# Kernel tuning notes

Hardware: AMD Instinct MI355X
Metric: run time of the kernel (lower is better)

Reference implementation:

```python
import jax, jax.numpy as jnp
import numpy as np

TEMPERATURE = 34.0
PAD = 1  # kernel_size // 2

def setup_inputs() -> dict:
    key = jax.random.key(0)
    ks = jax.random.split(key, 5)
    B, C, H, W = 32, 256, 56, 56
    K, O, I, kh = 4, 256, 256, 3
    hidden = int(C * 0.25) + 1  # 65
    return {
        "x": jax.random.normal(ks[0], (B, C, H, W), jnp.float32),
        "fc1_w": jax.random.normal(ks[1], (hidden, C), jnp.float32) * (2.0 / C) ** 0.5,
        "fc2_w": jax.random.normal(ks[2], (K, hidden), jnp.float32) * (2.0 / hidden) ** 0.5,
        "fc2_b": jnp.zeros((K,), jnp.float32),
        "weight": jax.random.normal(ks[3], (K, O, I, kh, kh), jnp.float32) * (2.0 / (I * kh * kh)) ** 0.5,
        "bias": jnp.zeros((K, O), jnp.float32),
    }

def reference(x, fc1_w, fc2_w, fc2_b, weight, bias):
    # attention2d: global avg pool -> 1x1 conv (fc1) -> relu -> 1x1 conv (fc2) -> softmax(logits/T)
    pooled = x.mean(axis=(2, 3))                      # [B, C]
    h = jax.nn.relu(pooled @ fc1_w.T)                 # [B, hidden]
    logits = h @ fc2_w.T + fc2_b                      # [B, K]
    att = jax.nn.softmax(logits / TEMPERATURE, axis=1)
    # aggregate per-sample conv weights/bias over K kernel banks
    agg_w = jnp.einsum('bk,koihw->boihw', att, weight)  # [B, O, I, kh, kw]
    agg_b = att @ bias                                  # [B, O]
    # per-sample conv (torch emulates via groups=B): vmap over batch
    def conv_one(xi, wi):
        return jax.lax.conv_general_dilated(
            xi[None], wi, window_strides=(1, 1),
            padding=((PAD, PAD), (PAD, PAD)),
            dimension_numbers=('NCHW', 'OIHW', 'NCHW'))[0]
    out = jax.vmap(conv_one)(x, agg_w)                 # [B, O, H, W]
    return out + agg_b[:, :, None, None]
```

## Files before the change

kernel.cpp:

```cpp
#include <hip/hip_runtime.h>


typedef short bf16x8 __attribute__((ext_vector_type(8)));
typedef float f32x16 __attribute__((ext_vector_type(16)));

__device__ __forceinline__ unsigned short f2bf(float f) {
  unsigned int u = __float_as_uint(f);
  return (unsigned short)((u + 0x7FFFu + ((u >> 16) & 1u)) >> 16);
}
__device__ __forceinline__ float bf2f(unsigned short h) {
  return __uint_as_float(((unsigned int)h) << 16);
}

__global__ void xcast_k(const float* __restrict__ x, unsigned short* __restrict__ xb,
                        float* __restrict__ pooled) {
  __shared__ __align__(16) unsigned short tile[64 * 260];
  int b = blockIdx.y;
  int hw0 = blockIdx.x * 64;
  int t = threadIdx.x;
  int lane = t & 63, wq = t >> 6;
#pragma unroll 8
  for (int it = 0; it < 64; ++it) {
    int c = it * 4 + wq;
    float v = x[((size_t)(b * 256 + c)) * 3136 + hw0 + lane];
    tile[lane * 260 + c] = f2bf(v);
  }
  __syncthreads();
  int c4 = lane * 4;
#pragma unroll
  for (int it = 0; it < 16; ++it) {
    int hl = it * 4 + wq;
    ushort4 v = *(const ushort4*)&tile[hl * 260 + c4];
    *(ushort4*)&xb[((size_t)(b * 3136 + hw0 + hl)) * 256 + c4] = v;
  }
  float s = 0.f;
#pragma unroll 16
  for (int hl = 0; hl < 64; ++hl) s += bf2f(tile[hl * 260 + t]);
  atomicAdd(&pooled[b * 256 + t], s * (1.0f / 3136.0f));
}

__global__ void att_k(const float* __restrict__ pooled, const float* __restrict__ fc1,
                      const float* __restrict__ fc2w, const float* __restrict__ fc2b,
                      const float* __restrict__ bias, float* __restrict__ att,
                      float* __restrict__ aggb) {
  int b = blockIdx.x, t = threadIdx.x;
  __shared__ float p[256];
  __shared__ float h[65];
  __shared__ float a4[4];
  for (int i = t; i < 256; i += 64) p[i] = pooled[b * 256 + i];
  __syncthreads();
  for (int j = t; j < 65; j += 64) {
    float s = 0.f;
    for (int c = 0; c < 256; ++c) s += p[c] * fc1[j * 256 + c];
    h[j] = fmaxf(s, 0.f);
  }
  __syncthreads();
  if (t == 0) {
    float lg[4];
    for (int k = 0; k < 4; ++k) {
      float s = fc2b[k];
      for (int j = 0; j < 65; ++j) s += h[j] * fc2w[k * 65 + j];
      lg[k] = s * (1.0f / 34.0f);
    }
    float m = fmaxf(fmaxf(lg[0], lg[1]), fmaxf(lg[2], lg[3]));
    float e0 = expf(lg[0] - m), e1 = expf(lg[1] - m), e2 = expf(lg[2] - m), e3 = expf(lg[3] - m);
    float inv = 1.0f / (e0 + e1 + e2 + e3);
    a4[0] = e0 * inv; a4[1] = e1 * inv; a4[2] = e2 * inv; a4[3] = e3 * inv;
    for (int k = 0; k < 4; ++k) att[b * 4 + k] = a4[k];
  }
  __syncthreads();
  for (int o = t; o < 256; o += 64) {
    float s = 0.f;
    for (int k = 0; k < 4; ++k) s += a4[k] * bias[k * 256 + o];
    aggb[b * 256 + o] = s;
  }
}

__global__ void aggw_k(const float* __restrict__ weight, const float* __restrict__ att,
                       unsigned short* __restrict__ aggw) {
  __shared__ float wl[4 * 2304];
  int o = blockIdx.x, t = threadIdx.x;
  for (int k = 0; k < 4; ++k)
    for (int idx = t; idx < 2304; idx += 256)
      wl[k * 2304 + idx] = weight[((size_t)(k * 256 + o)) * 2304 + idx];
  __syncthreads();
  int ot = o >> 6, ol = o & 63, ic = t >> 4, il = t & 15;
  for (int b = 0; b < 32; ++b) {
    float a0 = att[b * 4 + 0], a1 = att[b * 4 + 1], a2 = att[b * 4 + 2], a3 = att[b * 4 + 3];
    size_t base = ((size_t)((b * 4 + ot) * 16 + ic)) * 9216 + ol * 16 + il;
#pragma unroll
    for (int r = 0; r < 9; ++r) {
      float s = a0 * wl[t * 9 + r] + a1 * wl[2304 + t * 9 + r] +
                a2 * wl[4608 + t * 9 + r] + a3 * wl[6912 + t * 9 + r];
      aggw[base + r * 1024] = f2bf(s);
    }
  }
}

#define LDSA 16384

__global__ __launch_bounds__(256, 3) void conv_k(const unsigned short* __restrict__ xb,
                                                 const unsigned short* __restrict__ aggw,
                                                 const float* __restrict__ aggb,
                                                 float* __restrict__ out) {
  __shared__ __align__(16) unsigned char lds[16384 + 18432];
  const int t = threadIdx.x;
  const int wid = t >> 6;
  const int lane = t & 63;
  const int l31 = lane & 31;
  const int q = lane >> 5;

  int id = blockIdx.x;
  int wgid = (id & 7) * 208 + (id >> 3);
  int bn = wgid % 13;
  int rest = wgid / 13;
  int bo = rest & 3;
  int b = rest >> 2;

  const int o0 = bo * 64;
  const int n0 = bn * 256;
  const int h0 = n0 / 56;

  int bbase[2], nn[2], swz[2][3];
#pragma unroll
  for (int nf = 0; nf < 2; ++nf) {
    int n = n0 + wid * 64 + nf * 32 + l31;
    int h = n / 56, w = n - h * 56;
    nn[nf] = n;
    bbase[nf] = ((h - h0) * 64 + w) * 32 + q * 16;
#pragma unroll
    for (int dw = 0; dw < 3; ++dw) swz[nf][dw] = ((w + dw) & 7) << 4;
  }
  int abase[2];
#pragma unroll
  for (int mf = 0; mf < 2; ++mf) {
    int ol = mf * 32 + l31;
    abase[mf] = (LDSA + ol * 32 + q * 16) ^ ((ol & 7) << 4);
  }

  int xsrc[4], xdst[4];
#pragma unroll
  for (int j = 0; j < 4; ++j) {
    int idx = j * 256 + t;
    int pos = idx >> 1, sub = idx & 1;
    int row = pos >> 6, col = pos & 63;
    int hg = h0 - 1 + row, wg2 = col - 1;
    bool valid = (col >= 1 && col <= 56 && hg >= 0 && hg < 56);
    xsrc[j] = valid ? ((hg * 56 + wg2) * 512 + sub * 16) : -1;
    xdst[j] = (idx * 16) ^ ((pos & 7) << 4);
  }
  int adst[5];
#pragma unroll
  for (int j = 0; j < 5; ++j) {
    int idx = j * 256 + t;
    adst[j] = LDSA + ((idx * 16) ^ (((idx >> 1) & 7) << 4));
  }

  f32x16 acc[2][2];
#pragma unroll
  for (int i = 0; i < 2; ++i)
#pragma unroll
    for (int j = 0; j < 2; ++j)
#pragma unroll
      for (int e = 0; e < 16; ++e) acc[i][j][e] = 0.f;

  const char* xb_b = (const char*)xb + (size_t)b * 3136 * 512;
  const char* ag_c = (const char*)aggw + (size_t)(b * 4 + bo) * 16 * 18432;

  for (int ic = 0; ic < 16; ++ic) {
    __syncthreads();
#pragma unroll
    for (int j = 0; j < 4; ++j) {
      uint4 v = make_uint4(0u, 0u, 0u, 0u);
      if (xsrc[j] >= 0) v = *(const uint4*)(xb_b + xsrc[j] + ic * 32);
      *(uint4*)(lds + xdst[j]) = v;
    }
#pragma unroll
    for (int j = 0; j < 5; ++j) {
      int idx = j * 256 + t;
      if (j < 4 || t < 128) {
        uint4 v = *(const uint4*)(ag_c + (size_t)ic * 18432 + idx * 16);
        *(uint4*)(lds + adst[j]) = v;
      }
    }
    __syncthreads();
#pragma unroll
    for (int r = 0; r < 9; ++r) {
      const int dh = r / 3, dw = r % 3;
      bf16x8 a0 = *(const bf16x8*)(lds + abase[0] + r * 2048);
      bf16x8 a1 = *(const bf16x8*)(lds + abase[1] + r * 2048);
      bf16x8 b0 = *(const bf16x8*)(lds + ((bbase[0] + dh * 2048 + dw * 32) ^ swz[0][dw]));
      bf16x8 b1 = *(const bf16x8*)(lds + ((bbase[1] + dh * 2048 + dw * 32) ^ swz[1][dw]));
      acc[0][0] = __builtin_amdgcn_mfma_f32_32x32x16_bf16(a0, b0, acc[0][0], 0, 0, 0);
      acc[0][1] = __builtin_amdgcn_mfma_f32_32x32x16_bf16(a0, b1, acc[0][1], 0, 0, 0);
      acc[1][0] = __builtin_amdgcn_mfma_f32_32x32x16_bf16(a1, b0, acc[1][0], 0, 0, 0);
      acc[1][1] = __builtin_amdgcn_mfma_f32_32x32x16_bf16(a1, b1, acc[1][1], 0, 0, 0);
    }
  }

#pragma unroll
  for (int mf = 0; mf < 2; ++mf) {
#pragma unroll
    for (int nf = 0; nf < 2; ++nf) {
      int n = nn[nf];
      if (n < 3136) {
#pragma unroll
        for (int reg = 0; reg < 16; ++reg) {
          int o = o0 + mf * 32 + (reg & 3) + 8 * (reg >> 2) + 4 * q;
          out[((size_t)(b * 256 + o)) * 3136 + n] = acc[mf][nf][reg] + aggb[b * 256 + o];
        }
      }
    }
  }
}

extern "C" void kernel_launch(void* const* d_in, const int* in_sizes, int n_in,
                              void* d_out, int out_size, void* d_ws, size_t ws_size,
                              hipStream_t stream) {
  const float* x      = (const float*)d_in[0];
  const float* fc1    = (const float*)d_in[1];
  const float* fc2w   = (const float*)d_in[2];
  const float* fc2b   = (const float*)d_in[3];
  const float* weight = (const float*)d_in[4];
  const float* bias   = (const float*)d_in[5];
  float* out = (float*)d_out;

  char* ws = (char*)d_ws;
  float* pooled         = (float*)(ws);
  float* att            = (float*)(ws + 32768);
  float* aggb           = (float*)(ws + 33280);
  unsigned short* aggw  = (unsigned short*)(ws + 66048);
  unsigned short* xb    = (unsigned short*)(ws + 66048 + 37748736);

  hipMemsetAsync(pooled, 0, 32768, stream);
  xcast_k<<<dim3(49, 32), 256, 0, stream>>>(x, xb, pooled);
  att_k<<<32, 64, 0, stream>>>(pooled, fc1, fc2w, fc2b, bias, att, aggb);
  aggw_k<<<256, 256, 0, stream>>>(weight, att, aggw);
  conv_k<<<1664, 256, 0, stream>>>(xb, aggw, aggb, out);
}
```

Baseline: 224.4 us.

## Widen conv tile to 128 outputs, double-buffer input tile, read weights directly

The conv kernel now computes 128 output channels by 256 pixels per block, with a 2x2 wave layout. Each wave reads its weight fragments straight from global memory instead of staging them in LDS. The input tile is double-buffered in LDS, with the next channel slice prefetched into registers during the MFMA loop, which drops one barrier per iteration. The aggregated-weight layout and the aggw kernel are reorganized to match, and aggw now also splits the batch across the grid. Costs are higher register use (occupancy hint lowered from 3 to 2 blocks), half as many blocks, and A-operand loads exposed to global/L2 latency.

Result: slower. 232.5 us (+3.6%).

```diff
diff --git a/kernel.cpp b/kernel.cpp
--- a/kernel.cpp
+++ b/kernel.cpp
@@ -84,59 +84,54 @@
     for (int idx = t; idx < 2304; idx += 256)
       wl[k * 2304 + idx] = weight[((size_t)(k * 256 + o)) * 2304 + idx];
   __syncthreads();
-  int ot = o >> 6, ol = o & 63, ic = t >> 4, il = t & 15;
-  for (int b = 0; b < 32; ++b) {
+  int ot = o >> 7, ol = o & 127, ic = t >> 4, il = t & 15;
+  int b0 = blockIdx.y * 8;
+  for (int b = b0; b < b0 + 8; ++b) {
     float a0 = att[b * 4 + 0], a1 = att[b * 4 + 1], a2 = att[b * 4 + 2], a3 = att[b * 4 + 3];
-    size_t base = ((size_t)((b * 4 + ot) * 16 + ic)) * 9216 + ol * 16 + il;
+    size_t base = ((size_t)((b * 2 + ot) * 16 + ic)) * (9 * 2048) + ol * 16 + il;
 #pragma unroll
     for (int r = 0; r < 9; ++r) {
       float s = a0 * wl[t * 9 + r] + a1 * wl[2304 + t * 9 + r] +
                 a2 * wl[4608 + t * 9 + r] + a3 * wl[6912 + t * 9 + r];
-      aggw[base + r * 1024] = f2bf(s);
-    }
-  }
-}
-
-#define LDSA 16384
-
-__global__ __launch_bounds__(256, 3) void conv_k(const unsigned short* __restrict__ xb,
+      aggw[base + r * 2048] = f2bf(s);
+    }
+  }
+}
+
+#define XBUF 16384
+
+__global__ __launch_bounds__(256, 2) void conv_k(const unsigned short* __restrict__ xb,
                                                  const unsigned short* __restrict__ aggw,
                                                  const float* __restrict__ aggb,
                                                  float* __restrict__ out) {
-  __shared__ __align__(16) unsigned char lds[16384 + 18432];
+  __shared__ __align__(16) unsigned char lds[2 * XBUF];
   const int t = threadIdx.x;
-  const int wid = t >> 6;
-  const int lane = t & 63;
-  const int l31 = lane & 31;
-  const int q = lane >> 5;
+  const int wid = t >> 6, lane = t & 63, l31 = lane & 31, q = lane >> 5;
+  const int wo = wid >> 1, wn = wid & 1;
 
   int id = blockIdx.x;
-  int wgid = (id & 7) * 208 + (id >> 3);
+  int wgid = (id & 7) * 104 + (id >> 3);
   int bn = wgid % 13;
   int rest = wgid / 13;
-  int bo = rest & 3;
-  int b = rest >> 2;
-
-  const int o0 = bo * 64;
+  int b = rest >> 1, bo = rest & 1;
+
+  const int o0 = bo * 128;
   const int n0 = bn * 256;
   const int h0 = n0 / 56;
 
-  int bbase[2], nn[2], swz[2][3];
-#pragma unroll
-  for (int nf = 0; nf < 2; ++nf) {
-    int n = n0 + wid * 64 + nf * 32 + l31;
+  int bbase[4], nn[4], swz[4][3];
+#pragma unroll
+  for (int nf = 0; nf < 4; ++nf) {
+    int n = n0 + wn * 128 + nf * 32 + l31;
     int h = n / 56, w = n - h * 56;
     nn[nf] = n;
     bbase[nf] = ((h - h0) * 64 + w) * 32 + q * 16;
 #pragma unroll
     for (int dw = 0; dw < 3; ++dw) swz[nf][dw] = ((w + dw) & 7) << 4;
   }
-  int abase[2];
-#pragma unroll
-  for (int mf = 0; mf < 2; ++mf) {
-    int ol = mf * 32 + l31;
-    abase[mf] = (LDSA + ol * 32 + q * 16) ^ ((ol & 7) << 4);
-  }
+  int aoff[2];
+#pragma unroll
+  for (int mf = 0; mf < 2; ++mf) aoff[mf] = (wo * 64 + mf * 32 + l31) * 32 + q * 16;
 
   int xsrc[4], xdst[4];
 #pragma unroll
@@ -144,71 +139,76 @@
     int idx = j * 256 + t;
     int pos = idx >> 1, sub = idx & 1;
     int row = pos >> 6, col = pos & 63;
-    int hg = h0 - 1 + row, wg2 = col - 1;
+    int hg = h0 - 1 + row, wg = col - 1;
     bool valid = (col >= 1 && col <= 56 && hg >= 0 && hg < 56);
-    xsrc[j] = valid ? ((hg * 56 + wg2) * 512 + sub * 16) : -1;
+    xsrc[j] = valid ? ((hg * 56 + wg) * 512 + sub * 16) : -1;
     xdst[j] = (idx * 16) ^ ((pos & 7) << 4);
   }
-  int adst[5];
-#pragma unroll
-  for (int j = 0; j < 5; ++j) {
-    int idx = j * 256 + t;
-    adst[j] = LDSA + ((idx * 16) ^ (((idx >> 1) & 7) << 4));
-  }
-
-  f32x16 acc[2][2];
+
+  f32x16 acc[2][4];
 #pragma unroll
   for (int i = 0; i < 2; ++i)
 #pragma unroll
-    for (int j = 0; j < 2; ++j)
+    for (int j = 0; j < 4; ++j)
 #pragma unroll
       for (int e = 0; e < 16; ++e) acc[i][j][e] = 0.f;
 
   const char* xb_b = (const char*)xb + (size_t)b * 3136 * 512;
-  const char* ag_c = (const char*)aggw + (size_t)(b * 4 + bo) * 16 * 18432;
-
+  const char* ag_c = (const char*)aggw + (size_t)rest * 589824;
+
+#pragma unroll
+  for (int j = 0; j < 4; ++j) {
+    uint4 v = make_uint4(0u, 0u, 0u, 0u);
+    if (xsrc[j] >= 0) v = *(const uint4*)(xb_b + xsrc[j]);
+    *(uint4*)(lds + xdst[j]) = v;
+  }
+  __syncthreads();
+
+  int cur = 0;
   for (int ic = 0; ic < 16; ++ic) {
-    __syncthreads();
-#pragma unroll
-    for (int j = 0; j < 4; ++j) {
-      uint4 v = make_uint4(0u, 0u, 0u, 0u);
-      if (xsrc[j] >= 0) v = *(const uint4*)(xb_b + xsrc[j] + ic * 32);
-      *(uint4*)(lds + xdst[j]) = v;
-    }
-#pragma unroll
-    for (int j = 0; j < 5; ++j) {
-      int idx = j * 256 + t;
-      if (j < 4 || t < 128) {
-        uint4 v = *(const uint4*)(ag_c + (size_t)ic * 18432 + idx * 16);
-        *(uint4*)(lds + adst[j]) = v;
+    uint4 nv[4];
+    const bool more = (ic + 1 < 16);
+    if (more) {
+#pragma unroll
+      for (int j = 0; j < 4; ++j) {
+        uint4 v = make_uint4(0u, 0u, 0u, 0u);
+        if (xsrc[j] >= 0) v = *(const uint4*)(xb_b + xsrc[j] + (ic + 1) * 32);
+        nv[j] = v;
       }
     }
-    __syncthreads();
+    const unsigned char* xlds = lds + cur * XBUF;
+    const char* agc = ag_c + (size_t)ic * 36864;
 #pragma unroll
     for (int r = 0; r < 9; ++r) {
       const int dh = r / 3, dw = r % 3;
-      bf16x8 a0 = *(const bf16x8*)(lds + abase[0] + r * 2048);
-      bf16x8 a1 = *(const bf16x8*)(lds + abase[1] + r * 2048);
-      bf16x8 b0 = *(const bf16x8*)(lds + ((bbase[0] + dh * 2048 + dw * 32) ^ swz[0][dw]));
-      bf16x8 b1 = *(const bf16x8*)(lds + ((bbase[1] + dh * 2048 + dw * 32) ^ swz[1][dw]));
-      acc[0][0] = __builtin_amdgcn_mfma_f32_32x32x16_bf16(a0, b0, acc[0][0], 0, 0, 0);
-      acc[0][1] = __builtin_amdgcn_mfma_f32_32x32x16_bf16(a0, b1, acc[0][1], 0, 0, 0);
-      acc[1][0] = __builtin_amdgcn_mfma_f32_32x32x16_bf16(a1, b0, acc[1][0], 0, 0, 0);
-      acc[1][1] = __builtin_amdgcn_mfma_f32_32x32x16_bf16(a1, b1, acc[1][1], 0, 0, 0);
-    }
+      bf16x8 a0 = *(const bf16x8*)(agc + r * 4096 + aoff[0]);
+      bf16x8 a1 = *(const bf16x8*)(agc + r * 4096 + aoff[1]);
+#pragma unroll
+      for (int nf = 0; nf < 4; ++nf) {
+        bf16x8 bb = *(const bf16x8*)(xlds + ((bbase[nf] + dh * 2048 + dw * 32) ^ swz[nf][dw]));
+        acc[0][nf] = __builtin_amdgcn_mfma_f32_32x32x16_bf16(a0, bb, acc[0][nf], 0, 0, 0);
+        acc[1][nf] = __builtin_amdgcn_mfma_f32_32x32x16_bf16(a1, bb, acc[1][nf], 0, 0, 0);
+      }
+    }
+    if (more) {
+      unsigned char* dst = lds + (cur ^ 1) * XBUF;
+#pragma unroll
+      for (int j = 0; j < 4; ++j) *(uint4*)(dst + xdst[j]) = nv[j];
+      __syncthreads();
+    }
+    cur ^= 1;
   }
 
 #pragma unroll
   for (int mf = 0; mf < 2; ++mf) {
 #pragma unroll
-    for (int nf = 0; nf < 2; ++nf) {
-      int n = nn[nf];
-      if (n < 3136) {
-#pragma unroll
-        for (int reg = 0; reg < 16; ++reg) {
-          int o = o0 + mf * 32 + (reg & 3) + 8 * (reg >> 2) + 4 * q;
-          out[((size_t)(b * 256 + o)) * 3136 + n] = acc[mf][nf][reg] + aggb[b * 256 + o];
-        }
+    for (int reg = 0; reg < 16; ++reg) {
+      int o = o0 + wo * 64 + mf * 32 + (reg & 3) + 8 * (reg >> 2) + 4 * q;
+      float ab = aggb[b * 256 + o];
+      float* op = out + ((size_t)(b * 256 + o)) * 3136;
+#pragma unroll
+      for (int nf = 0; nf < 4; ++nf) {
+        if (nn[nf] < 3136) op[nn[nf]] = acc[mf][nf][reg] + ab;
       }
     }
   }
@@ -235,6 +235,6 @@
   hipMemsetAsync(pooled, 0, 32768, stream);
   xcast_k<<<dim3(49, 32), 256, 0, stream>>>(x, xb, pooled);
   att_k<<<32, 64, 0, stream>>>(pooled, fc1, fc2w, fc2b, bias, att, aggb);
-  aggw_k<<<256, 256, 0, stream>>>(weight, att, aggw);
-  conv_k<<<1664, 256, 0, stream>>>(xb, aggw, aggb, out);
-}
+  aggw_k<<<dim3(256, 4), 256, 0, stream>>>(weight, att, aggw);
+  conv_k<<<832, 256, 0, stream>>>(xb, aggw, aggb, out);
+}
```
